# Optimization experiments

Measured on AMD Instinct MI355X. Metric: run time of the kernel, lower is better.

## Reference

```python
import jax, jax.numpy as jnp
import numpy as np

B, N, H = 8, 256, 256


def setup_inputs() -> dict:
    key = jax.random.key(0)
    ks = jax.random.split(key, 6)
    s = 1.0 / np.sqrt(H)
    return {
        "x": jax.random.normal(ks[0], (B, N, H), dtype=jnp.float32),
        "edge_gate": jax.random.uniform(ks[1], (B, N, N, H), dtype=jnp.float32),
        "U_w": jax.random.uniform(ks[2], (H, H), jnp.float32, -s, s),
        "U_b": jax.random.uniform(ks[3], (H,), jnp.float32, -s, s),
        "V_w": jax.random.uniform(ks[4], (H, H), jnp.float32, -s, s),
        "V_b": jax.random.uniform(ks[5], (H,), jnp.float32, -s, s),
    }


def reference(x, edge_gate, U_w, U_b, V_w, V_b):
    # Ux, Vx: (B, N, H); torch Linear computes x @ W.T + b
    Ux = jnp.einsum("bnh,kh->bnk", x, U_w) + U_b
    Vx = jnp.einsum("bnh,kh->bnk", x, V_w) + V_b
    # sum_j edge_gate[b,i,j,h] * Vx[b,j,h]  -> (B, N, H), fused (no gateVx materialized)
    num = jnp.einsum("bijh,bjh->bih", edge_gate, Vx)
    denom = 1e-20 + jnp.sum(edge_gate, axis=2)  # (B, N, H)
    return Ux + num / denom
```

## Files before the change

kernel.cpp:

```cpp
#include <hip/hip_runtime.h>


#define LDS_STRIDE 72

__global__ __launch_bounds__(256) void gemm_uv(
    const float* __restrict__ x, const float* __restrict__ U_w,
    const float* __restrict__ U_b, const float* __restrict__ V_w,
    const float* __restrict__ V_b, float* __restrict__ C) {
  __shared__ float Xs[32 * LDS_STRIDE];
  __shared__ float Ws[32 * LDS_STRIDE];
  const int t  = threadIdx.x;
  const int gx = blockIdx.x;
  const int gy = blockIdx.y;
  const int n0 = gx * 64;
  const int m0 = gy * 64;
  const float* Wsrc  = (gx < 4) ? U_w : V_w;
  const float* bsrc  = (gx < 4) ? U_b : V_b;
  const int    nbase = (gx < 4) ? n0  : n0 - 256;
  const int tn = t & 15;
  const int tm = t >> 4;
  float acc[4][4] = {};

  for (int k0 = 0; k0 < 256; k0 += 32) {
    #pragma unroll
    for (int rep = 0; rep < 2; ++rep) {
      const int f  = t + rep * 256;
      const int rl = f >> 3;
      const int h4 = f & 7;
      float4 xa = *(const float4*)(x    + (m0    + rl) * 256 + k0 + h4 * 4);
      float4 wa = *(const float4*)(Wsrc + (nbase + rl) * 256 + k0 + h4 * 4);
      Xs[(h4 * 4 + 0) * LDS_STRIDE + rl] = xa.x;
      Xs[(h4 * 4 + 1) * LDS_STRIDE + rl] = xa.y;
      Xs[(h4 * 4 + 2) * LDS_STRIDE + rl] = xa.z;
      Xs[(h4 * 4 + 3) * LDS_STRIDE + rl] = xa.w;
      Ws[(h4 * 4 + 0) * LDS_STRIDE + rl] = wa.x;
      Ws[(h4 * 4 + 1) * LDS_STRIDE + rl] = wa.y;
      Ws[(h4 * 4 + 2) * LDS_STRIDE + rl] = wa.z;
      Ws[(h4 * 4 + 3) * LDS_STRIDE + rl] = wa.w;
    }
    __syncthreads();
    #pragma unroll
    for (int kk = 0; kk < 32; ++kk) {
      float4 a = *(const float4*)(&Xs[kk * LDS_STRIDE + tm * 4]);
      float4 b = *(const float4*)(&Ws[kk * LDS_STRIDE + tn * 4]);
      float av[4] = {a.x, a.y, a.z, a.w};
      float bv[4] = {b.x, b.y, b.z, b.w};
      #pragma unroll
      for (int i = 0; i < 4; ++i)
        #pragma unroll
        for (int j = 0; j < 4; ++j)
          acc[i][j] += av[i] * bv[j];
    }
    __syncthreads();
  }

  const float4 bias = *(const float4*)(bsrc + nbase + tn * 4);
  const float bv[4] = {bias.x, bias.y, bias.z, bias.w};
  #pragma unroll
  for (int i = 0; i < 4; ++i) {
    float4 o;
    o.x = acc[i][0] + bv[0];
    o.y = acc[i][1] + bv[1];
    o.z = acc[i][2] + bv[2];
    o.w = acc[i][3] + bv[3];
    *(float4*)(C + (m0 + tm * 4 + i) * 512 + n0 + tn * 4) = o;
  }
}

__global__ __launch_bounds__(256) void fuse_gate(
    const float* __restrict__ eg, const float* __restrict__ C,
    float* __restrict__ out) {
  const int i  = blockIdx.x;
  const int b  = blockIdx.y;
  const int t  = threadIdx.x;
  const int h4 = t & 63;
  const int jg = t >> 6;

  const float4* eg4 = (const float4*)eg;
  const float4* C4  = (const float4*)C;

  const int row_bi = b * 256 + i;
  const int eg_base = row_bi * (256 * 64);
  const int vx_base = b * 256 * 128 + 64;

  float4 num = {0.f, 0.f, 0.f, 0.f};
  float4 den = {0.f, 0.f, 0.f, 0.f};
  for (int j = jg; j < 256; j += 4) {
    float4 e = eg4[eg_base + j * 64 + h4];
    float4 v = C4[vx_base + j * 128 + h4];
    num.x += e.x * v.x;  num.y += e.y * v.y;
    num.z += e.z * v.z;  num.w += e.w * v.w;
    den.x += e.x;  den.y += e.y;
    den.z += e.z;  den.w += e.w;
  }

  __shared__ float4 nsh[256];
  __shared__ float4 dsh[256];
  nsh[t] = num;
  dsh[t] = den;
  __syncthreads();

  if (t < 64) {
    float4 ns = nsh[t];
    float4 ds = dsh[t];
    #pragma unroll
    for (int g = 1; g < 4; ++g) {
      float4 nn = nsh[g * 64 + t];
      float4 dd = dsh[g * 64 + t];
      ns.x += nn.x; ns.y += nn.y; ns.z += nn.z; ns.w += nn.w;
      ds.x += dd.x; ds.y += dd.y; ds.z += dd.z; ds.w += dd.w;
    }
    float4 u = C4[row_bi * 128 + t];
    float4 o;
    o.x = u.x + ns.x / (1e-20f + ds.x);
    o.y = u.y + ns.y / (1e-20f + ds.y);
    o.z = u.z + ns.z / (1e-20f + ds.z);
    o.w = u.w + ns.w / (1e-20f + ds.w);
    ((float4*)out)[row_bi * 64 + t] = o;
  }
}

extern "C" void kernel_launch(void* const* d_in, const int* in_sizes, int n_in,
                              void* d_out, int out_size, void* d_ws, size_t ws_size,
                              hipStream_t stream) {
  const float* x   = (const float*)d_in[0];
  const float* eg  = (const float*)d_in[1];
  const float* U_w = (const float*)d_in[2];
  const float* U_b = (const float*)d_in[3];
  const float* V_w = (const float*)d_in[4];
  const float* V_b = (const float*)d_in[5];
  float* out = (float*)d_out;
  float* C   = (float*)d_ws;

  gemm_uv<<<dim3(8, 32), 256, 0, stream>>>(x, U_w, U_b, V_w, V_b, C);
  fuse_gate<<<dim3(256, 8), 256, 0, stream>>>(eg, C, out);
}
```

Measured before the change: 716.2 us.

## Split Ux/Vx outputs, retile GEMM, use nontemporal edge-gate loads

The GEMM now writes Ux straight into the output buffer and Vx into a compact workspace, launching twice as many blocks with 64x32 tiles and a K-contiguous LDS layout. The gate kernel reads Vx with a tighter stride, streams edge_gate through nontemporal loads, unrolls the j loop, and reads Ux back from the output. The intent is better cache behaviour for the dominant edge_gate stream and a GEMM that fills more of the device. The cost is a read-modify-write of the output buffer, which relies on the GEMM finishing before the gate kernel runs.

```diff
diff --git a/kernel.cpp b/kernel.cpp
--- a/kernel.cpp
+++ b/kernel.cpp
@@ -1,74 +1,80 @@
 #include <hip/hip_runtime.h>
 
 
-#define LDS_STRIDE 72
+typedef float f4 __attribute__((ext_vector_type(4)));
+typedef float f2 __attribute__((ext_vector_type(2)));
+
+#define S36 36
 
 __global__ __launch_bounds__(256) void gemm_uv(
     const float* __restrict__ x, const float* __restrict__ U_w,
     const float* __restrict__ U_b, const float* __restrict__ V_w,
-    const float* __restrict__ V_b, float* __restrict__ C) {
-  __shared__ float Xs[32 * LDS_STRIDE];
-  __shared__ float Ws[32 * LDS_STRIDE];
+    const float* __restrict__ V_b, float* __restrict__ Ux,
+    float* __restrict__ Vx) {
+  __shared__ float Xs[64 * S36];
+  __shared__ float Ws[32 * S36];
   const int t  = threadIdx.x;
   const int gx = blockIdx.x;
   const int gy = blockIdx.y;
-  const int n0 = gx * 64;
   const int m0 = gy * 64;
-  const float* Wsrc  = (gx < 4) ? U_w : V_w;
-  const float* bsrc  = (gx < 4) ? U_b : V_b;
-  const int    nbase = (gx < 4) ? n0  : n0 - 256;
+  const bool isU = (gx < 8);
+  const float* Wsrc = isU ? U_w : V_w;
+  const float* bsrc = isU ? U_b : V_b;
+  const int n0 = (gx & 7) * 32;
+  float* dst = isU ? Ux : Vx;
+
   const int tn = t & 15;
   const int tm = t >> 4;
-  float acc[4][4] = {};
+  float acc[4][2] = {};
+
+  const int lm = t >> 3;
+  const int lc = t & 7;
 
   for (int k0 = 0; k0 < 256; k0 += 32) {
     #pragma unroll
-    for (int rep = 0; rep < 2; ++rep) {
-      const int f  = t + rep * 256;
-      const int rl = f >> 3;
-      const int h4 = f & 7;
-      float4 xa = *(const float4*)(x    + (m0    + rl) * 256 + k0 + h4 * 4);
-      float4 wa = *(const float4*)(Wsrc + (nbase + rl) * 256 + k0 + h4 * 4);
-      Xs[(h4 * 4 + 0) * LDS_STRIDE + rl] = xa.x;
-      Xs[(h4 * 4 + 1) * LDS_STRIDE + rl] = xa.y;
-      Xs[(h4 * 4 + 2) * LDS_STRIDE + rl] = xa.z;
-      Xs[(h4 * 4 + 3) * LDS_STRIDE + rl] = xa.w;
-      Ws[(h4 * 4 + 0) * LDS_STRIDE + rl] = wa.x;
-      Ws[(h4 * 4 + 1) * LDS_STRIDE + rl] = wa.y;
-      Ws[(h4 * 4 + 2) * LDS_STRIDE + rl] = wa.z;
-      Ws[(h4 * 4 + 3) * LDS_STRIDE + rl] = wa.w;
+    for (int r = 0; r < 2; ++r) {
+      const int m = r * 32 + lm;
+      f4 v = *(const f4*)(x + (m0 + m) * 256 + k0 + lc * 4);
+      *(f4*)(&Xs[m * S36 + lc * 4]) = v;
+    }
+    {
+      f4 v = *(const f4*)(Wsrc + (n0 + lm) * 256 + k0 + lc * 4);
+      *(f4*)(&Ws[lm * S36 + lc * 4]) = v;
     }
     __syncthreads();
     #pragma unroll
-    for (int kk = 0; kk < 32; ++kk) {
-      float4 a = *(const float4*)(&Xs[kk * LDS_STRIDE + tm * 4]);
-      float4 b = *(const float4*)(&Ws[kk * LDS_STRIDE + tn * 4]);
-      float av[4] = {a.x, a.y, a.z, a.w};
-      float bv[4] = {b.x, b.y, b.z, b.w};
-      #pragma unroll
-      for (int i = 0; i < 4; ++i)
-        #pragma unroll
-        for (int j = 0; j < 4; ++j)
-          acc[i][j] += av[i] * bv[j];
+    for (int kq = 0; kq < 8; ++kq) {
+      f4 a0 = *(const f4*)(&Xs[(tm * 4 + 0) * S36 + kq * 4]);
+      f4 a1 = *(const f4*)(&Xs[(tm * 4 + 1) * S36 + kq * 4]);
+      f4 a2 = *(const f4*)(&Xs[(tm * 4 + 2) * S36 + kq * 4]);
+      f4 a3 = *(const f4*)(&Xs[(tm * 4 + 3) * S36 + kq * 4]);
+      f4 b0 = *(const f4*)(&Ws[(tn * 2 + 0) * S36 + kq * 4]);
+      f4 b1 = *(const f4*)(&Ws[(tn * 2 + 1) * S36 + kq * 4]);
+      acc[0][0] += a0.x*b0.x + a0.y*b0.y + a0.z*b0.z + a0.w*b0.w;
+      acc[0][1] += a0.x*b1.x + a0.y*b1.y + a0.z*b1.z + a0.w*b1.w;
+      acc[1][0] += a1.x*b0.x + a1.y*b0.y + a1.z*b0.z + a1.w*b0.w;
+      acc[1][1] += a1.x*b1.x + a1.y*b1.y + a1.z*b1.z + a1.w*b1.w;
+      acc[2][0] += a2.x*b0.x + a2.y*b0.y + a2.z*b0.z + a2.w*b0.w;
+      acc[2][1] += a2.x*b1.x + a2.y*b1.y + a2.z*b1.z + a2.w*b1.w;
+      acc[3][0] += a3.x*b0.x + a3.y*b0.y + a3.z*b0.z + a3.w*b0.w;
+      acc[3][1] += a3.x*b1.x + a3.y*b1.y + a3.z*b1.z + a3.w*b1.w;
     }
     __syncthreads();
   }
 
-  const float4 bias = *(const float4*)(bsrc + nbase + tn * 4);
-  const float bv[4] = {bias.x, bias.y, bias.z, bias.w};
+  const float bb0 = bsrc[n0 + 2 * tn + 0];
+  const float bb1 = bsrc[n0 + 2 * tn + 1];
   #pragma unroll
   for (int i = 0; i < 4; ++i) {
-    float4 o;
-    o.x = acc[i][0] + bv[0];
-    o.y = acc[i][1] + bv[1];
-    o.z = acc[i][2] + bv[2];
-    o.w = acc[i][3] + bv[3];
-    *(float4*)(C + (m0 + tm * 4 + i) * 512 + n0 + tn * 4) = o;
+    f2 o;
+    o.x = acc[i][0] + bb0;
+    o.y = acc[i][1] + bb1;
+    *(f2*)(dst + (m0 + 4 * tm + i) * 256 + n0 + 2 * tn) = o;
   }
 }
 
 __global__ __launch_bounds__(256) void fuse_gate(
-    const float* __restrict__ eg, const float* __restrict__ C,
+    const float* __restrict__ eg, const float* __restrict__ Vx,
     float* __restrict__ out) {
   const int i  = blockIdx.x;
   const int b  = blockIdx.y;
@@ -76,47 +82,37 @@
   const int h4 = t & 63;
   const int jg = t >> 6;
 
-  const float4* eg4 = (const float4*)eg;
-  const float4* C4  = (const float4*)C;
+  const f4* eg4 = (const f4*)eg;
+  const f4* vx4 = (const f4*)Vx;
+  const int row = b * 256 + i;
+  const int egb = row * (256 * 64);
+  const int vxb = b * (256 * 64);
 
-  const int row_bi = b * 256 + i;
-  const int eg_base = row_bi * (256 * 64);
-  const int vx_base = b * 256 * 128 + 64;
-
-  float4 num = {0.f, 0.f, 0.f, 0.f};
-  float4 den = {0.f, 0.f, 0.f, 0.f};
+  f4 num = {0.f, 0.f, 0.f, 0.f};
+  f4 den = {0.f, 0.f, 0.f, 0.f};
+  #pragma unroll 4
   for (int j = jg; j < 256; j += 4) {
-    float4 e = eg4[eg_base + j * 64 + h4];
-    float4 v = C4[vx_base + j * 128 + h4];
-    num.x += e.x * v.x;  num.y += e.y * v.y;
-    num.z += e.z * v.z;  num.w += e.w * v.w;
-    den.x += e.x;  den.y += e.y;
-    den.z += e.z;  den.w += e.w;
+    f4 e = __builtin_nontemporal_load(&eg4[egb + j * 64 + h4]);
+    f4 v = vx4[vxb + j * 64 + h4];
+    num += e * v;
+    den += e;
   }
 
-  __shared__ float4 nsh[256];
-  __shared__ float4 dsh[256];
+  __shared__ f4 nsh[256];
+  __shared__ f4 dsh[256];
   nsh[t] = num;
   dsh[t] = den;
   __syncthreads();
 
   if (t < 64) {
-    float4 ns = nsh[t];
-    float4 ds = dsh[t];
+    f4 ns = nsh[t];
+    f4 ds = dsh[t];
     #pragma unroll
-    for (int g = 1; g < 4; ++g) {
-      float4 nn = nsh[g * 64 + t];
-      float4 dd = dsh[g * 64 + t];
-      ns.x += nn.x; ns.y += nn.y; ns.z += nn.z; ns.w += nn.w;
-      ds.x += dd.x; ds.y += dd.y; ds.z += dd.z; ds.w += dd.w;
-    }
-    float4 u = C4[row_bi * 128 + t];
-    float4 o;
-    o.x = u.x + ns.x / (1e-20f + ds.x);
-    o.y = u.y + ns.y / (1e-20f + ds.y);
-    o.z = u.z + ns.z / (1e-20f + ds.z);
-    o.w = u.w + ns.w / (1e-20f + ds.w);
-    ((float4*)out)[row_bi * 64 + t] = o;
+    for (int g = 1; g < 4; ++g) { ns += nsh[g * 64 + t]; ds += dsh[g * 64 + t]; }
+    f4 u = ((const f4*)out)[row * 64 + t];
+    f4 eps = {1e-20f, 1e-20f, 1e-20f, 1e-20f};
+    f4 o = u + ns / (eps + ds);
+    ((f4*)out)[row * 64 + t] = o;
   }
 }
 
@@ -130,8 +126,8 @@
   const float* V_w = (const float*)d_in[4];
   const float* V_b = (const float*)d_in[5];
   float* out = (float*)d_out;
-  float* C   = (float*)d_ws;
+  float* Vx  = (float*)d_ws;
 
-  gemm_uv<<<dim3(8, 32), 256, 0, stream>>>(x, U_w, U_b, V_w, V_b, C);
-  fuse_gate<<<dim3(256, 8), 256, 0, stream>>>(eg, C, out);
+  gemm_uv<<<dim3(16, 32), 256, 0, stream>>>(x, U_w, U_b, V_w, V_b, out, Vx);
+  fuse_gate<<<dim3(256, 8), 256, 0, stream>>>(eg, Vx, out);
 }
```

New measurement: 686.6 us. 4.1% less time.
